# Performance work log

Measured on AMD Instinct MI355X. Metric: run time of the kernel, lower is better.

The kernel has to match this reference:

```python
import jax, jax.numpy as jnp
import numpy as np
import math

B = 2048
STEP = 2        # candidate restarts (original hardcodes 100)
DDIM = 20       # DDIM reverse steps
TIME_DIM = 512
STATE = 6
ACT = 8


def _ddim_coeffs():
    # noise schedule from sample_backward (numpy, host-side constants)
    T = 1000
    t = np.arange(1, T + 1, dtype=np.float64)
    b_max, b_min = 10.0, 0.1
    alpha = np.exp(-b_min / T - 0.5 * (b_max - b_min) * (2 * t - 1) / T ** 2)
    ap = np.cumprod(alpha)
    ts = np.linspace(T, 0, DDIM + 1).astype(np.int64)
    coeffs = []
    for i in range(1, DDIM + 1):
        cur = int(ts[i - 1] - 1)
        prev = int(ts[i] - 1)
        ab_c = ap[cur]
        ab_p = ap[prev] if prev >= 0 else 1.0
        c1 = (ab_p / ab_c) ** 0.5
        var = (1 - ab_p) / (1 - ab_c) * (1 - ab_c / ab_p)  # eta=1 (simple_var)
        c2 = max(1 - ab_p - var, 0.0) ** 0.5 - (ab_p * (1 - ab_c) / ab_c) ** 0.5
        c3 = (1 - ab_c / ab_p) ** 0.5                      # simple_var third term
        coeffs.append((float(cur), float(c1), float(c2), float(c3)))
    return coeffs

_COEFFS = _ddim_coeffs()

_PI = math.pi
JOINT_HIGH = np.array([35 * _PI / 180, -60 * _PI / 180, 3.94, 155 * _PI / 180,
                       -55 * _PI / 180, _PI, 5 * _PI / 180, 3.71], dtype=np.float32)
JOINT_LOW = np.array([-35 * _PI / 180, -155 * _PI / 180, 2.59, 60 * _PI / 180,
                      -125 * _PI / 180, -_PI, -90 * _PI / 180, 2.50], dtype=np.float32)


def _time_emb(cur_t):
    # sinusoidal encoding of a scalar timestep, interleaved sin/cos -> [TIME_DIM]
    div = jnp.exp(jnp.arange(0, TIME_DIM, 2, dtype=jnp.float32) * (-math.log(10000.0) / TIME_DIM))
    return jnp.stack([jnp.sin(cur_t * div), jnp.cos(cur_t * div)], axis=1).reshape(-1)


def _fk(joints):
    # DH forward kinematics over 8 joints; joints: [B, 8] -> pose [B, 6]
    q1, q2, d3, q4, q5, q6, q7, d8 = (joints[:, k] for k in range(8))
    zeros = jnp.zeros_like(q1)
    ones = jnp.ones_like(q1)
    alpha = jnp.deg2rad(jnp.array([0., -90., -90., 90., -90., -90., 90., -90.], dtype=jnp.float32))
    a = jnp.array([0., 0.16, 0.07, 0., 0.1334, 0., 0.15, 0.3625], dtype=jnp.float32)
    d = jnp.stack([zeros, zeros, d3, zeros, -0.1316 * ones, 1.0105 * ones, 0.52 * ones, d8], axis=1)  # [B,8]
    th = jnp.stack([q1, q2, zeros, q4, q5, q6, q7, zeros], axis=1)  # [B,8]
    ct, st = jnp.cos(th), jnp.sin(th)
    ca, sa = jnp.cos(alpha), jnp.sin(alpha)  # [8]
    z8 = jnp.zeros_like(ct)
    o8 = jnp.ones_like(ct)
    ab = jnp.broadcast_to(a, ct.shape)
    row0 = jnp.stack([ct, -st, z8, ab], axis=-1)
    row1 = jnp.stack([st * ca, ct * ca, -sa * o8, -sa * d], axis=-1)
    row2 = jnp.stack([st * sa, ct * sa, ca * o8, ca * d], axis=-1)
    row3 = jnp.stack([z8, z8, z8, o8], axis=-1)
    M = jnp.stack([row0, row1, row2, row3], axis=2)  # [B, 8, 4, 4]
    T = M[:, 0]
    for j in range(1, 8):  # fixed tiny chain of 7 bmms
        T = T @ M[:, j]
    R = T[:, :3, :3]
    hole = jnp.array([0., 0., 3.75], dtype=jnp.float32)
    e1 = R @ hole  # [B, 3]
    pose = jnp.stack([T[:, 0, 3], T[:, 1, 3], T[:, 2, 3] + 1.702,
                      e1[:, 0] + T[:, 0, 3], e1[:, 1] + T[:, 1, 3], e1[:, 2] + T[:, 2, 3] + 1.702], axis=1)
    return pose


def setup_inputs() -> dict:
    key = jax.random.key(0)
    ks = jax.random.split(key, 16)

    def w(k, i, o):
        return jax.random.normal(k, (i, o), jnp.float32) / float(np.sqrt(i))

    return {
        "x_pre": jax.random.normal(ks[0], (B, STATE), jnp.float32) * 50.0,
        "noise": jax.random.normal(ks[1], (STEP, B, ACT), jnp.float32),
        "W_in": w(ks[2], STATE + ACT + TIME_DIM, 512), "b_in": jnp.zeros((512,), jnp.float32),
        "W1": w(ks[3], 512, 512), "b1": jnp.zeros((512,), jnp.float32),
        "W2": w(ks[4], 512, 512), "b2": jnp.zeros((512,), jnp.float32),
        "W3": w(ks[5], 512, 512), "b3": jnp.zeros((512,), jnp.float32),
        "W4": w(ks[6], 512, 512), "b4": jnp.zeros((512,), jnp.float32),
        "W_out": w(ks[7], 512, ACT), "b_out": jnp.zeros((ACT,), jnp.float32),
    }


def reference(x_pre, noise, W_in, b_in, W1, b1, W2, b2, W3, b3, W4, b4, W_out, b_out):
    gelu = lambda v: jax.nn.gelu(v, approximate=False)

    def denoiser(state, action, cur_t):
        t_emb = jnp.broadcast_to(_time_emb(cur_t), (state.shape[0], TIME_DIM))
        x = jnp.concatenate([state, action, t_emb], axis=1)
        y = gelu(x @ W_in + b_in)
        y = gelu(y @ W1 + b1)
        y = gelu(y @ W2 + b2)
        y = gelu(y @ W3 + b3)
        y = gelu(y @ W4 + b4)
        return y @ W_out + b_out

    high = jnp.asarray(JOINT_HIGH)
    low = jnp.asarray(JOINT_LOW)

    errors, joints_all = [], []
    for s in range(STEP):
        nz = noise[s]
        # DDIM reverse loop; NB: the original never feeds z back into `noise`,
        # so each iteration denoises the same initial noise (replicated faithfully).
        z = nz
        for (cur_t, c1, c2, c3) in _COEFFS:
            joint_0 = denoiser(x_pre, nz, cur_t)
            z = c1 * nz + c2 * joint_0 + c3 * nz
        joint_normal = (jnp.tanh(z / 10.0) + 1.0) / 2.0
        new_joint = joint_normal * (high - low) + low  # [B, 8]
        pose_V = _fk(new_joint)                         # [B, 6]
        moni = 100.0 * pose_V
        dist0 = jnp.sqrt(jnp.sum((moni[:, :3] - x_pre[:, :3]) ** 2, axis=1))
        dist1 = jnp.sqrt(jnp.sum((moni[:, 3:] - x_pre[:, 3:]) ** 2, axis=1))
        errors.append(dist0 + dist1)
        joints_all.append(new_joint)

    errors = jnp.stack(errors, axis=0)        # [STEP, B]
    joints_all = jnp.stack(joints_all, axis=0)  # [STEP, B, 8]
    idx = jnp.argmin(errors, axis=0)          # per-sample best restart
    best = jnp.take_along_axis(joints_all, idx[None, :, None], axis=0)[0]  # [B, 8]
    return best
```

## Files before the change

### kernel.cpp

```cpp
#include <hip/hip_runtime.h>
#include <math.h>

typedef __bf16 bf16x8 __attribute__((ext_vector_type(8)));
typedef float f32x4 __attribute__((ext_vector_type(4)));
typedef unsigned short u16;
typedef unsigned short u16x8 __attribute__((ext_vector_type(8)));
typedef unsigned int u32;

constexpr int BATCH = 2048;
constexpr int ROWS  = 4096;
constexpr int HID   = 512;
constexpr int NACT  = 8;

__device__ __forceinline__ float gelu_f(float x) {
    return 0.5f * x * (1.0f + erff(x * 0.70710678118654752f));
}
__device__ __forceinline__ u16 f2bf(float f) {
    u32 u = __float_as_uint(f);
    return (u16)((u + 0x7FFFu + ((u >> 16) & 1u)) >> 16);
}
__device__ __forceinline__ float bf2f(u16 h) {
    return __uint_as_float(((u32)h) << 16);
}

__device__ __forceinline__ size_t fragoff(int r, int k) {
    return (size_t)(((r >> 4) * 16 + (k >> 5)) * 512
                    + (((k & 31) >> 3) * 16 + (r & 15)) * 8 + (k & 7));
}

__global__ __launch_bounds__(256) void k_prep(
        const float* __restrict__ W1, const float* __restrict__ W2,
        const float* __restrict__ W3, const float* __restrict__ W4,
        const float* __restrict__ W_in,
        u16* __restrict__ wt, float* __restrict__ partials) {
    int z = blockIdx.z;
    if (z == 4) {
        if (blockIdx.x >= 4 || blockIdx.y != 0) return;
        __shared__ float temb[128];
        int x = blockIdx.x, t = threadIdx.x;
        if (t < 128) {
            int k = x * 128 + t;
            int p = k >> 1;
            float div = expf((float)(2 * p) * (-9.210340371976184f / 512.0f));
            temb[t] = (k & 1) ? cosf(49.0f * div) : sinf(49.0f * div);
        }
        __syncthreads();
#pragma unroll
        for (int half = 0; half < 2; ++half) {
            int col = half * 256 + t;
            float acc = 0.f;
            for (int kk = 0; kk < 128; ++kk)
                acc += temb[kk] * W_in[(size_t)(14 + x * 128 + kk) * HID + col];
            partials[x * HID + col] = acc;
        }
        return;
    }
    __shared__ float tile[32][33];
    const float* Ws[4] = {W1, W2, W3, W4};
    const float* W = Ws[z];
    u16* wh = wt + (size_t)z * 524288;
    u16* wl = wh + 262144;
    int kt = blockIdx.x * 32, nt = blockIdx.y * 32, t = threadIdx.x;
    int c = t & 31, r = t >> 5;
#pragma unroll
    for (int p = 0; p < 4; ++p)
        tile[r + p * 8][c] = W[(size_t)(kt + r + p * 8) * HID + nt + c];
    __syncthreads();
#pragma unroll
    for (int p = 0; p < 4; ++p) {
        int nl = r + p * 8, kl = c;
        float v = tile[kl][nl];
        u16 h = f2bf(v);
        u16 l2 = f2bf(v - bf2f(h));
        size_t o = fragoff(nt + nl, kt + kl);
        wh[o] = h;
        wl[o] = l2;
    }
}

__global__ __launch_bounds__(256) void k_layer_in(
        const float* __restrict__ x_pre, const float* __restrict__ noise,
        const float* __restrict__ W_in, const float* __restrict__ b_in,
        const float* __restrict__ partials,
        u16* __restrict__ Yh, u16* __restrict__ Yl) {
    int id = blockIdx.x * 256 + threadIdx.x;
    int r = id >> 6, oct = id & 63;
    int s = r >> 11, bidx = r & 2047;
    float xv[6], nz[8];
#pragma unroll
    for (int j = 0; j < 6; ++j) xv[j] = x_pre[bidx * 6 + j];
#pragma unroll
    for (int j = 0; j < 8; ++j) nz[j] = noise[(s * BATCH + bidx) * NACT + j];
    int nc = oct * 8;
    float acc[8];
#pragma unroll
    for (int q = 0; q < 2; ++q) {
        float4 bv = *(const float4*)&b_in[nc + q * 4];
        float4 p0 = *(const float4*)&partials[nc + q * 4];
        float4 p1 = *(const float4*)&partials[512 + nc + q * 4];
        float4 p2 = *(const float4*)&partials[1024 + nc + q * 4];
        float4 p3 = *(const float4*)&partials[1536 + nc + q * 4];
        acc[q * 4 + 0] = bv.x + p0.x + p1.x + p2.x + p3.x;
        acc[q * 4 + 1] = bv.y + p0.y + p1.y + p2.y + p3.y;
        acc[q * 4 + 2] = bv.z + p0.z + p1.z + p2.z + p3.z;
        acc[q * 4 + 3] = bv.w + p0.w + p1.w + p2.w + p3.w;
    }
#pragma unroll
    for (int j = 0; j < 14; ++j) {
        float xj = (j < 6) ? xv[j] : nz[j - 6];
        float4 wa = *(const float4*)&W_in[j * HID + nc];
        float4 wb = *(const float4*)&W_in[j * HID + nc + 4];
        acc[0] += xj * wa.x; acc[1] += xj * wa.y;
        acc[2] += xj * wa.z; acc[3] += xj * wa.w;
        acc[4] += xj * wb.x; acc[5] += xj * wb.y;
        acc[6] += xj * wb.z; acc[7] += xj * wb.w;
    }
    u16x8 hv, lv;
#pragma unroll
    for (int j2 = 0; j2 < 8; ++j2) {
        float g = gelu_f(acc[j2]);
        u16 hi = f2bf(g);
        hv[j2] = hi;
        lv[j2] = f2bf(g - bf2f(hi));
    }
    size_t o = fragoff(r, nc);
    *(u16x8*)&Yh[o] = hv;
    *(u16x8*)&Yl[o] = lv;
}

__global__ __launch_bounds__(256) void k_gemm_f(
        const u16* __restrict__ Ah, const u16* __restrict__ Al,
        const u16* __restrict__ Wh, const u16* __restrict__ Wl,
        const float* __restrict__ bias,
        u16* __restrict__ Yh, u16* __restrict__ Yl) {
    __shared__ __align__(16) u16 lds[3][20][512];
    int tid = threadIdx.x, lane = tid & 63, w = tid >> 6;
    int m0 = blockIdx.x * 32, n0 = blockIdx.y * 128;

    int apl = w >> 1, ag = w & 1;
    const u16* aplane = apl ? Al : Ah;
    const u16* srcA = aplane + (size_t)((blockIdx.x * 2 + ag) * 16) * 512 + lane * 8;
    const u16* srcB0 = Wh + (size_t)((blockIdx.y * 8 + 2 * w) * 16) * 512 + lane * 8;
    const u16* srcB1 = Wh + (size_t)((blockIdx.y * 8 + 2 * w + 1) * 16) * 512 + lane * 8;
    const u16* srcB2 = Wl + (size_t)((blockIdx.y * 8 + 2 * w) * 16) * 512 + lane * 8;
    const u16* srcB3 = Wl + (size_t)((blockIdx.y * 8 + 2 * w + 1) * 16) * 512 + lane * 8;

    auto stage = [&](int c, int sl) {
        __builtin_amdgcn_global_load_lds(
            (const __attribute__((address_space(1))) void*)(srcA + c * 512),
            (__attribute__((address_space(3))) void*)&lds[sl][apl * 2 + ag][0], 16, 0, 0);
        __builtin_amdgcn_global_load_lds(
            (const __attribute__((address_space(1))) void*)(srcB0 + c * 512),
            (__attribute__((address_space(3))) void*)&lds[sl][4 + 2 * w][0], 16, 0, 0);
        __builtin_amdgcn_global_load_lds(
            (const __attribute__((address_space(1))) void*)(srcB1 + c * 512),
            (__attribute__((address_space(3))) void*)&lds[sl][4 + 2 * w + 1][0], 16, 0, 0);
        __builtin_amdgcn_global_load_lds(
            (const __attribute__((address_space(1))) void*)(srcB2 + c * 512),
            (__attribute__((address_space(3))) void*)&lds[sl][12 + 2 * w][0], 16, 0, 0);
        __builtin_amdgcn_global_load_lds(
            (const __attribute__((address_space(1))) void*)(srcB3 + c * 512),
            (__attribute__((address_space(3))) void*)&lds[sl][12 + 2 * w + 1][0], 16, 0, 0);
    };

    f32x4 zero = {0.f, 0.f, 0.f, 0.f};
    f32x4 acc[2][2] = {{zero, zero}, {zero, zero}};

    stage(0, 0);
    stage(1, 1);
#pragma unroll
    for (int c = 0; c < 16; ++c) {
        int sl = c % 3;
        if (c < 15) { asm volatile("s_waitcnt vmcnt(5)" ::: "memory"); }
        else        { asm volatile("s_waitcnt vmcnt(0)" ::: "memory"); }
        __builtin_amdgcn_s_barrier();
        __builtin_amdgcn_sched_barrier(0);

        bf16x8 ah[2], al[2], bh[2], bl[2];
#pragma unroll
        for (int i = 0; i < 2; ++i) {
            ah[i] = *(const bf16x8*)&lds[sl][i][lane * 8];
            al[i] = *(const bf16x8*)&lds[sl][2 + i][lane * 8];
        }
#pragma unroll
        for (int j = 0; j < 2; ++j) {
            bh[j] = *(const bf16x8*)&lds[sl][4 + 2 * w + j][lane * 8];
            bl[j] = *(const bf16x8*)&lds[sl][12 + 2 * w + j][lane * 8];
        }
        __builtin_amdgcn_s_setprio(1);
#pragma unroll
        for (int i = 0; i < 2; ++i)
#pragma unroll
            for (int j = 0; j < 2; ++j) {
                acc[i][j] = __builtin_amdgcn_mfma_f32_16x16x32_bf16(ah[i], bh[j], acc[i][j], 0, 0, 0);
                acc[i][j] = __builtin_amdgcn_mfma_f32_16x16x32_bf16(ah[i], bl[j], acc[i][j], 0, 0, 0);
                acc[i][j] = __builtin_amdgcn_mfma_f32_16x16x32_bf16(al[i], bh[j], acc[i][j], 0, 0, 0);
            }
        __builtin_amdgcn_s_setprio(0);
        __builtin_amdgcn_sched_barrier(0);
        if (c < 14) stage(c + 2, (c + 2) % 3);
    }

#pragma unroll
    for (int i = 0; i < 2; ++i) {
        int row0 = m0 + i * 16 + (lane >> 4) * 4;
#pragma unroll
        for (int j = 0; j < 2; ++j) {
            int col = n0 + w * 32 + j * 16 + (lane & 15);
            float bia = bias[col];
#pragma unroll
            for (int r2 = 0; r2 < 4; ++r2) {
                float g = gelu_f(acc[i][j][r2] + bia);
                u16 hi = f2bf(g);
                size_t o = fragoff(row0 + r2, col);
                Yh[o] = hi;
                Yl[o] = f2bf(g - bf2f(hi));
            }
        }
    }
}

__device__ void mat4mul(float C[4][4], const float A[4][4], const float Bm[4][4]) {
#pragma unroll
    for (int i = 0; i < 4; ++i)
#pragma unroll
        for (int j = 0; j < 4; ++j) {
            float s = A[i][0] * Bm[0][j];
            s += A[i][1] * Bm[1][j];
            s += A[i][2] * Bm[2][j];
            s += A[i][3] * Bm[3][j];
            C[i][j] = s;
        }
}

__global__ __launch_bounds__(256) void k_out_fk(
        const u16* __restrict__ Yh, const u16* __restrict__ Yl,
        const float* __restrict__ W_out, const float* __restrict__ b_out,
        const float* __restrict__ noise, const float* __restrict__ x_pre,
        float* __restrict__ out, float c1, float c2, float c3) {
    int b = blockIdx.x * 4 + (threadIdx.x >> 6);
    int lane = threadIdx.x & 63;

    float acc0[8] = {0, 0, 0, 0, 0, 0, 0, 0};
    float acc1[8] = {0, 0, 0, 0, 0, 0, 0, 0};
#pragma unroll
    for (int it = 0; it < 8; ++it) {
        int k = lane + it * 64;
        size_t o0 = fragoff(b, k);
        size_t o1 = fragoff(BATCH + b, k);
        float ya = bf2f(Yh[o0]) + bf2f(Yl[o0]);
        float yb = bf2f(Yh[o1]) + bf2f(Yl[o1]);
        float4 w0 = ((const float4*)&W_out[k * NACT])[0];
        float4 w1 = ((const float4*)&W_out[k * NACT])[1];
        acc0[0] += ya * w0.x; acc0[1] += ya * w0.y; acc0[2] += ya * w0.z; acc0[3] += ya * w0.w;
        acc0[4] += ya * w1.x; acc0[5] += ya * w1.y; acc0[6] += ya * w1.z; acc0[7] += ya * w1.w;
        acc1[0] += yb * w0.x; acc1[1] += yb * w0.y; acc1[2] += yb * w0.z; acc1[3] += yb * w0.w;
        acc1[4] += yb * w1.x; acc1[5] += yb * w1.y; acc1[6] += yb * w1.z; acc1[7] += yb * w1.w;
    }
#pragma unroll
    for (int n = 0; n < 8; ++n) {
#pragma unroll
        for (int off = 32; off > 0; off >>= 1) {
            acc0[n] += __shfl_xor(acc0[n], off, 64);
            acc1[n] += __shfl_xor(acc1[n], off, 64);
        }
    }

    float jq[8] = {0, 0, 0, 0, 0, 0, 0, 0};
    float err = 0.f;
    if (lane < 2) {
        int s = lane;
        const float* accp = (s == 0) ? acc0 : acc1;
        const float HIf[8] = {
            (float)(35.0 * M_PI / 180.0), (float)(-60.0 * M_PI / 180.0), 3.94f,
            (float)(155.0 * M_PI / 180.0), (float)(-55.0 * M_PI / 180.0),
            (float)M_PI, (float)(5.0 * M_PI / 180.0), 3.71f};
        const float LOf[8] = {
            (float)(-35.0 * M_PI / 180.0), (float)(-155.0 * M_PI / 180.0), 2.59f,
            (float)(60.0 * M_PI / 180.0), (float)(-125.0 * M_PI / 180.0),
            (float)(-M_PI), (float)(-90.0 * M_PI / 180.0), 2.5f};
        const float* nzp = &noise[(s * BATCH + b) * NACT];
#pragma unroll
        for (int n = 0; n < 8; ++n) {
            float o = accp[n] + b_out[n];
            float z = c1 * nzp[n] + c2 * o + c3 * nzp[n];
            float jn = (tanhf(z * 0.1f) + 1.0f) * 0.5f;
            jq[n] = jn * (HIf[n] - LOf[n]) + LOf[n];
        }
        const float a_[8]  = {0.0f, 0.16f, 0.07f, 0.0f, 0.1334f, 0.0f, 0.15f, 0.3625f};
        const float ca_[8] = {1.f, 0.f, 0.f, 0.f, 0.f, 0.f, 0.f, 0.f};
        const float sa_[8] = {0.f, -1.f, -1.f, 1.f, -1.f, -1.f, 1.f, -1.f};
        float d_[8] = {0.0f, 0.0f, jq[2], 0.0f, -0.1316f, 1.0105f, 0.52f, jq[7]};
        float th[8] = {jq[0], jq[1], 0.0f, jq[3], jq[4], jq[5], jq[6], 0.0f};
        float T[4][4], M[4][4], Tn[4][4];
#pragma unroll
        for (int j = 0; j < 8; ++j) {
            float ct = cosf(th[j]);
            float st = sinf(th[j]);
            M[0][0] = ct;          M[0][1] = -st;         M[0][2] = 0.0f;    M[0][3] = a_[j];
            M[1][0] = st * ca_[j]; M[1][1] = ct * ca_[j]; M[1][2] = -sa_[j]; M[1][3] = -sa_[j] * d_[j];
            M[2][0] = st * sa_[j]; M[2][1] = ct * sa_[j]; M[2][2] = ca_[j];  M[2][3] = ca_[j] * d_[j];
            M[3][0] = 0.0f;        M[3][1] = 0.0f;        M[3][2] = 0.0f;    M[3][3] = 1.0f;
            if (j == 0) {
#pragma unroll
                for (int i = 0; i < 4; ++i)
#pragma unroll
                    for (int cc = 0; cc < 4; ++cc) T[i][cc] = M[i][cc];
            } else {
                mat4mul(Tn, T, M);
#pragma unroll
                for (int i = 0; i < 4; ++i)
#pragma unroll
                    for (int cc = 0; cc < 4; ++cc) T[i][cc] = Tn[i][cc];
            }
        }
        float e1x = T[0][2] * 3.75f;
        float e1y = T[1][2] * 3.75f;
        float e1z = T[2][2] * 3.75f;
        float p0 = T[0][3];
        float p1 = T[1][3];
        float p2 = T[2][3] + 1.702f;
        float p3 = e1x + T[0][3];
        float p4 = e1y + T[1][3];
        float p5 = e1z + T[2][3] + 1.702f;
        const float* xp = &x_pre[b * 6];
        float dx0 = 100.0f * p0 - xp[0];
        float dx1 = 100.0f * p1 - xp[1];
        float dx2 = 100.0f * p2 - xp[2];
        float dx3 = 100.0f * p3 - xp[3];
        float dx4 = 100.0f * p4 - xp[4];
        float dx5 = 100.0f * p5 - xp[5];
        err = sqrtf(dx0 * dx0 + dx1 * dx1 + dx2 * dx2) +
              sqrtf(dx3 * dx3 + dx4 * dx4 + dx5 * dx5);
    }
    float e0 = __shfl(err, 0, 64);
    float e1 = __shfl(err, 1, 64);
    int sel = (e1 < e0) ? 1 : 0;
    float jsel[8];
#pragma unroll
    for (int n = 0; n < 8; ++n) jsel[n] = __shfl(jq[n], sel, 64);
    if (lane == 0) {
#pragma unroll
        for (int n = 0; n < 8; ++n) out[b * NACT + n] = jsel[n];
    }
}

extern "C" void kernel_launch(void* const* d_in, const int* in_sizes, int n_in,
                              void* d_out, int out_size, void* d_ws, size_t ws_size,
                              hipStream_t stream) {
    const float* x_pre = (const float*)d_in[0];
    const float* noise = (const float*)d_in[1];
    const float* W_in  = (const float*)d_in[2];
    const float* b_in  = (const float*)d_in[3];
    const float* W1    = (const float*)d_in[4];
    const float* b1    = (const float*)d_in[5];
    const float* W2    = (const float*)d_in[6];
    const float* b2    = (const float*)d_in[7];
    const float* W3    = (const float*)d_in[8];
    const float* b3    = (const float*)d_in[9];
    const float* W4    = (const float*)d_in[10];
    const float* b4    = (const float*)d_in[11];
    const float* W_out = (const float*)d_in[12];
    const float* b_out = (const float*)d_in[13];

    double ab_c = exp(-0.1 * 50.0 / 1000.0 - 0.5 * (10.0 - 0.1) * 2500.0 / 1.0e6);
    float c1 = (float)sqrt(1.0 / ab_c);
    float c2 = (float)(-sqrt((1.0 - ab_c) / ab_c));
    float c3 = (float)sqrt(1.0 - ab_c);

    char* base = (char*)d_ws;
    u16* Ah = (u16*)base;
    u16* Al = Ah + 2097152;
    u16* Bh = Al + 2097152;
    u16* Bl = Bh + 2097152;
    u16* wt = (u16*)(base + 16777216);
    float* partials = (float*)(base + 16777216 + 4194304);

    k_prep<<<dim3(16, 16, 5), 256, 0, stream>>>(W1, W2, W3, W4, W_in, wt, partials);
    k_layer_in<<<ROWS * 64 / 256, 256, 0, stream>>>(x_pre, noise, W_in, b_in,
                                                    partials, Ah, Al);
    dim3 g(ROWS / 32, HID / 128);
    k_gemm_f<<<g, 256, 0, stream>>>(Ah, Al, wt + 0 * 524288, wt + 0 * 524288 + 262144, b1, Bh, Bl);
    k_gemm_f<<<g, 256, 0, stream>>>(Bh, Bl, wt + 1 * 524288, wt + 1 * 524288 + 262144, b2, Ah, Al);
    k_gemm_f<<<g, 256, 0, stream>>>(Ah, Al, wt + 2 * 524288, wt + 2 * 524288 + 262144, b3, Bh, Bl);
    k_gemm_f<<<g, 256, 0, stream>>>(Bh, Bl, wt + 3 * 524288, wt + 3 * 524288 + 262144, b4, Ah, Al);
    k_out_fk<<<BATCH / 4, 256, 0, stream>>>(Ah, Al, W_out, b_out, noise, x_pre,
                                            (float*)d_out, c1, c2, c3);
}
```

Before: 93.89 us.

## Retile split-bf16 GEMM to 64x64 blocks with intra-block split-K reduction

The hidden-layer GEMM changes from 32x128 tiles with 4 waves to 64x64 tiles with 8 waves. The waves are split into two K halves that each process 8 K-chunks, and their partial accumulators are reduced through LDS at the end. The pipeline goes from triple to double buffering, issuing the next stage's loads before waiting. The aim is to balance A and W reuse and to shorten each wave's serial K loop. In exchange it adds an LDS reduction, two block-wide syncs, and leaves half the waves idle during the epilogue.

Result: faster. 90.62 us (-3.5%).

```diff
diff --git a/kernel.cpp b/kernel.cpp
--- a/kernel.cpp
+++ b/kernel.cpp
@@ -128,64 +128,65 @@
     *(u16x8*)&Yl[o] = lv;
 }
 
-__global__ __launch_bounds__(256) void k_gemm_f(
+__global__ __launch_bounds__(512) void k_gemm_f(
         const u16* __restrict__ Ah, const u16* __restrict__ Al,
         const u16* __restrict__ Wh, const u16* __restrict__ Wl,
         const float* __restrict__ bias,
         u16* __restrict__ Yh, u16* __restrict__ Yl) {
-    __shared__ __align__(16) u16 lds[3][20][512];
+    __shared__ __align__(16) u16 lds[2][2][16][512];
     int tid = threadIdx.x, lane = tid & 63, w = tid >> 6;
-    int m0 = blockIdx.x * 32, n0 = blockIdx.y * 128;
-
-    int apl = w >> 1, ag = w & 1;
-    const u16* aplane = apl ? Al : Ah;
-    const u16* srcA = aplane + (size_t)((blockIdx.x * 2 + ag) * 16) * 512 + lane * 8;
-    const u16* srcB0 = Wh + (size_t)((blockIdx.y * 8 + 2 * w) * 16) * 512 + lane * 8;
-    const u16* srcB1 = Wh + (size_t)((blockIdx.y * 8 + 2 * w + 1) * 16) * 512 + lane * 8;
-    const u16* srcB2 = Wl + (size_t)((blockIdx.y * 8 + 2 * w) * 16) * 512 + lane * 8;
-    const u16* srcB3 = Wl + (size_t)((blockIdx.y * 8 + 2 * w + 1) * 16) * 512 + lane * 8;
-
-    auto stage = [&](int c, int sl) {
+    int q = w & 3, kh = w >> 2;
+    int qr = q >> 1, qc = q & 1;
+    int m0 = blockIdx.x * 64, n0 = blockIdx.y * 64;
+
+    int a0 = 2 * q, a1 = 2 * q + 1;
+    int apl0 = a0 >> 2, ag0 = a0 & 3, apl1 = a1 >> 2, ag1 = a1 & 3;
+    const u16* srcA0 = (apl0 ? Al : Ah) + (size_t)((blockIdx.x * 4 + ag0) * 16 + kh * 8) * 512 + lane * 8;
+    const u16* srcA1 = (apl1 ? Al : Ah) + (size_t)((blockIdx.x * 4 + ag1) * 16 + kh * 8) * 512 + lane * 8;
+    const u16* srcB0 = (apl0 ? Wl : Wh) + (size_t)((blockIdx.y * 4 + ag0) * 16 + kh * 8) * 512 + lane * 8;
+    const u16* srcB1 = (apl1 ? Wl : Wh) + (size_t)((blockIdx.y * 4 + ag1) * 16 + kh * 8) * 512 + lane * 8;
+
+    auto stage = [&](int s, int sl) {
         __builtin_amdgcn_global_load_lds(
-            (const __attribute__((address_space(1))) void*)(srcA + c * 512),
-            (__attribute__((address_space(3))) void*)&lds[sl][apl * 2 + ag][0], 16, 0, 0);
+            (const __attribute__((address_space(1))) void*)(srcA0 + s * 512),
+            (__attribute__((address_space(3))) void*)&lds[sl][kh][a0][0], 16, 0, 0);
         __builtin_amdgcn_global_load_lds(
-            (const __attribute__((address_space(1))) void*)(srcB0 + c * 512),
-            (__attribute__((address_space(3))) void*)&lds[sl][4 + 2 * w][0], 16, 0, 0);
+            (const __attribute__((address_space(1))) void*)(srcA1 + s * 512),
+            (__attribute__((address_space(3))) void*)&lds[sl][kh][a1][0], 16, 0, 0);
         __builtin_amdgcn_global_load_lds(
-            (const __attribute__((address_space(1))) void*)(srcB1 + c * 512),
-            (__attribute__((address_space(3))) void*)&lds[sl][4 + 2 * w + 1][0], 16, 0, 0);
+            (const __attribute__((address_space(1))) void*)(srcB0 + s * 512),
+            (__attribute__((address_space(3))) void*)&lds[sl][kh][8 + a0][0], 16, 0, 0);
         __builtin_amdgcn_global_load_lds(
-            (const __attribute__((address_space(1))) void*)(srcB2 + c * 512),
-            (__attribute__((address_space(3))) void*)&lds[sl][12 + 2 * w][0], 16, 0, 0);
-        __builtin_amdgcn_global_load_lds(
-            (const __attribute__((address_space(1))) void*)(srcB3 + c * 512),
-            (__attribute__((address_space(3))) void*)&lds[sl][12 + 2 * w + 1][0], 16, 0, 0);
+            (const __attribute__((address_space(1))) void*)(srcB1 + s * 512),
+            (__attribute__((address_space(3))) void*)&lds[sl][kh][8 + a1][0], 16, 0, 0);
     };
 
     f32x4 zero = {0.f, 0.f, 0.f, 0.f};
     f32x4 acc[2][2] = {{zero, zero}, {zero, zero}};
 
     stage(0, 0);
-    stage(1, 1);
-#pragma unroll
-    for (int c = 0; c < 16; ++c) {
-        int sl = c % 3;
-        if (c < 15) { asm volatile("s_waitcnt vmcnt(5)" ::: "memory"); }
-        else        { asm volatile("s_waitcnt vmcnt(0)" ::: "memory"); }
+#pragma unroll
+    for (int s = 0; s < 8; ++s) {
+        int sl = s & 1;
+        if (s < 7) {
+            stage(s + 1, sl ^ 1);
+            asm volatile("s_waitcnt vmcnt(4)" ::: "memory");
+        } else {
+            asm volatile("s_waitcnt vmcnt(0)" ::: "memory");
+        }
         __builtin_amdgcn_s_barrier();
         __builtin_amdgcn_sched_barrier(0);
 
         bf16x8 ah[2], al[2], bh[2], bl[2];
 #pragma unroll
         for (int i = 0; i < 2; ++i) {
-            ah[i] = *(const bf16x8*)&lds[sl][i][lane * 8];
-            al[i] = *(const bf16x8*)&lds[sl][2 + i][lane * 8];
+            ah[i] = *(const bf16x8*)&lds[sl][kh][qr * 2 + i][lane * 8];
+            al[i] = *(const bf16x8*)&lds[sl][kh][4 + qr * 2 + i][lane * 8];
         }
 #pragma unroll
         for (int j = 0; j < 2; ++j) {
-            bh[j] = *(const bf16x8*)&lds[sl][4 + 2 * w + j][lane * 8];
-            bl[j] = *(const bf16x8*)&lds[sl][12 + 2 * w + j][lane * 8];
+            bh[j] = *(const bf16x8*)&lds[sl][kh][8 + qc * 2 + j][lane * 8];
+            bl[j] = *(const bf16x8*)&lds[sl][kh][12 + qc * 2 + j][lane * 8];
         }
         __builtin_amdgcn_s_setprio(1);
 #pragma unroll
@@ -198,23 +199,37 @@
             }
         __builtin_amdgcn_s_setprio(0);
         __builtin_amdgcn_sched_barrier(0);
-        if (c < 14) stage(c + 2, (c + 2) % 3);
-    }
-
-#pragma unroll
-    for (int i = 0; i < 2; ++i) {
-        int row0 = m0 + i * 16 + (lane >> 4) * 4;
-#pragma unroll
-        for (int j = 0; j < 2; ++j) {
-            int col = n0 + w * 32 + j * 16 + (lane & 15);
-            float bia = bias[col];
-#pragma unroll
-            for (int r2 = 0; r2 < 4; ++r2) {
-                float g = gelu_f(acc[i][j][r2] + bia);
-                u16 hi = f2bf(g);
-                size_t o = fragoff(row0 + r2, col);
-                Yh[o] = hi;
-                Yl[o] = f2bf(g - bf2f(hi));
+    }
+
+    __syncthreads();
+    float* red = (float*)&lds[0][0][0][0];
+    if (kh == 1) {
+#pragma unroll
+        for (int f = 0; f < 4; ++f)
+            *(f32x4*)&red[(q * 64 + lane) * 16 + f * 4] = acc[f >> 1][f & 1];
+    }
+    __syncthreads();
+    if (kh == 0) {
+#pragma unroll
+        for (int f = 0; f < 4; ++f) {
+            f32x4 p = *(const f32x4*)&red[(q * 64 + lane) * 16 + f * 4];
+            acc[f >> 1][f & 1] += p;
+        }
+#pragma unroll
+        for (int i = 0; i < 2; ++i) {
+            int row0 = m0 + qr * 32 + i * 16 + (lane >> 4) * 4;
+#pragma unroll
+            for (int j = 0; j < 2; ++j) {
+                int col = n0 + qc * 32 + j * 16 + (lane & 15);
+                float bia = bias[col];
+#pragma unroll
+                for (int r2 = 0; r2 < 4; ++r2) {
+                    float g = gelu_f(acc[i][j][r2] + bia);
+                    u16 hi = f2bf(g);
+                    size_t o = fragoff(row0 + r2, col);
+                    Yh[o] = hi;
+                    Yl[o] = f2bf(g - bf2f(hi));
+                }
             }
         }
     }
@@ -379,11 +394,11 @@
     k_prep<<<dim3(16, 16, 5), 256, 0, stream>>>(W1, W2, W3, W4, W_in, wt, partials);
     k_layer_in<<<ROWS * 64 / 256, 256, 0, stream>>>(x_pre, noise, W_in, b_in,
                                                     partials, Ah, Al);
-    dim3 g(ROWS / 32, HID / 128);
-    k_gemm_f<<<g, 256, 0, stream>>>(Ah, Al, wt + 0 * 524288, wt + 0 * 524288 + 262144, b1, Bh, Bl);
-    k_gemm_f<<<g, 256, 0, stream>>>(Bh, Bl, wt + 1 * 524288, wt + 1 * 524288 + 262144, b2, Ah, Al);
-    k_gemm_f<<<g, 256, 0, stream>>>(Ah, Al, wt + 2 * 524288, wt + 2 * 524288 + 262144, b3, Bh, Bl);
-    k_gemm_f<<<g, 256, 0, stream>>>(Bh, Bl, wt + 3 * 524288, wt + 3 * 524288 + 262144, b4, Ah, Al);
+    dim3 g(ROWS / 64, HID / 64);
+    k_gemm_f<<<g, 512, 0, stream>>>(Ah, Al, wt + 0 * 524288, wt + 0 * 524288 + 262144, b1, Bh, Bl);
+    k_gemm_f<<<g, 512, 0, stream>>>(Bh, Bl, wt + 1 * 524288, wt + 1 * 524288 + 262144, b2, Ah, Al);
+    k_gemm_f<<<g, 512, 0, stream>>>(Ah, Al, wt + 2 * 524288, wt + 2 * 524288 + 262144, b3, Bh, Bl);
+    k_gemm_f<<<g, 512, 0, stream>>>(Bh, Bl, wt + 3 * 524288, wt + 3 * 524288 + 262144, b4, Ah, Al);
     k_out_fk<<<BATCH / 4, 256, 0, stream>>>(Ah, Al, W_out, b_out, noise, x_pre,
                                             (float*)d_out, c1, c2, c3);
 }
```
